# Kernel tuning notes

Hardware: AMD Instinct MI355X
Metric: run time of the kernel (lower is better)

Reference implementation:

```python
import jax, jax.numpy as jnp
import numpy as np

N_USERS = 200000
N_ITEMS = 50000
F = 64          # n_factors
B = 32768       # batch of (user, item) pairs
L = 256         # ratings per user (dense-ified ragged lists)
MIN_R = 1
MAX_R = 5


def setup_inputs() -> dict:
    key = jax.random.key(0)
    ks = jax.random.split(key, 8)
    # xavier_normal_ std = sqrt(2 / (fan_in + fan_out))
    std_u = (2.0 / (N_USERS + F)) ** 0.5
    std_i = (2.0 / (N_ITEMS + F)) ** 0.5
    user_factors = jax.random.normal(ks[0], (N_USERS, F), dtype=jnp.float32) * std_u
    item_factors = jax.random.normal(ks[1], (N_ITEMS, F), dtype=jnp.float32) * std_i
    user_biases = jax.random.normal(ks[2], (N_USERS, 1), dtype=jnp.float32)
    item_biases = jax.random.normal(ks[3], (N_ITEMS, 1), dtype=jnp.float32)
    # integer star ratings in [MIN_R, MAX_R], one dense row per user
    ratings = jax.random.randint(ks[4], (N_USERS, L), MIN_R, MAX_R + 1).astype(jnp.float32)
    users = jax.random.randint(ks[5], (B,), 0, N_USERS)
    items = jax.random.randint(ks[6], (B,), 0, N_ITEMS)
    item_pos = jax.random.randint(ks[7], (B,), 0, L)  # position of the item in the user's rating row
    return {
        "users": users, "items": items, "item_pos": item_pos,
        "ratings": ratings,
        "user_factors": user_factors, "item_factors": item_factors,
        "user_biases": user_biases, "item_biases": item_biases,
        "min_rating": MIN_R, "max_rating": MAX_R,
    }


def reference(users, items, item_pos, ratings, user_factors, item_factors,
              user_biases, item_biases, min_rating, max_rating):
    b = users.shape[0]
    # MF prediction: biases + dot(user_factor, item_factor), shape [B, 1]
    pred = (user_biases[users] + item_biases[items]
            + jnp.sum(user_factors[users] * item_factors[items], axis=1, keepdims=True))
    p = pred[:, 0]  # [B]

    # per-sample: user's rating row with this item's rating replaced by the prediction
    rows = ratings[users]                                   # [B, L]
    rows = rows.at[jnp.arange(b), item_pos].set(p)          # batched index-update

    # torch.histc(bins=max_rating, min=min_rating, max=max_rating):
    # width = (max - min) / bins; values outside [min, max] ignored; x == max -> last bin
    bins = max_rating
    width = (max_rating - min_rating) / bins
    idx = jnp.floor((rows - min_rating) / width)
    idx = jnp.where(rows == max_rating, bins - 1, idx)      # [B, L]
    in_range = (rows >= min_rating) & (rows <= max_rating)

    # end bin from rounded prediction: clip(round(p), max(min-1, 0), max-1)
    end = jnp.clip(jnp.round(p), max(min_rating - 1, 0), max_rating - 1)  # [B]

    # mass = sum(hist[0:end+1]) - 0.5 * hist[end]  == count(idx<=end) - 0.5*count(idx==end)
    le = jnp.where(in_range & (idx <= end[:, None]), 1.0, 0.0)
    eq = jnp.where(in_range & (idx == end[:, None]), 1.0, 0.0)
    mass = jnp.sum(le - 0.5 * eq, axis=1, keepdims=True)    # [B, 1]

    return jnp.stack((pred, mass), axis=1)                   # [B, 2, 1]
```

## Files before the change

### kernel.cpp

```cpp
#include <hip/hip_runtime.h>

__global__ __launch_bounds__(256) void hist_mf_kernel(
    const int*   __restrict__ users,
    const int*   __restrict__ items,
    const int*   __restrict__ item_pos,
    const float* __restrict__ ratings,
    const float* __restrict__ user_factors,
    const float* __restrict__ item_factors,
    const float* __restrict__ user_biases,
    const float* __restrict__ item_biases,
    const int*   __restrict__ minr_p,
    const int*   __restrict__ maxr_p,
    int L, int F, int B,
    float* __restrict__ out)
{
    const int wavesPerBlock = blockDim.x >> 6;
    const int wave = blockIdx.x * wavesPerBlock + (threadIdx.x >> 6);
    const int lane = threadIdx.x & 63;
    if (wave >= B) return;

    const int u   = users[wave];
    const int it  = items[wave];
    const int pos = item_pos[wave];

    const int   minr = *minr_p;
    const int   maxr = *maxr_p;
    const int   bins = maxr;
    const float fmin = (float)minr;
    const float fmax = (float)maxr;
    const float width = (float)(maxr - minr) / (float)bins;
    const float lo = (float)((minr - 1) > 0 ? (minr - 1) : 0);
    const float hi = (float)(maxr - 1);

    float d = 0.f;
    for (int f = lane; f < F; f += 64)
        d += user_factors[(size_t)u * F + f] * item_factors[(size_t)it * F + f];
    #pragma unroll
    for (int o = 32; o > 0; o >>= 1) d += __shfl_xor(d, o, 64);

    const float pred = user_biases[u] + item_biases[it] + d;
    const float end  = fminf(fmaxf(rintf(pred), lo), hi);

    const float* row = ratings + (size_t)u * L;
    float mass = 0.f;

    for (int base = 0; base < (L & ~255); base += 256) {
        float4 r4 = reinterpret_cast<const float4*>(row + base)[lane];
        float rv[4] = {r4.x, r4.y, r4.z, r4.w};
        #pragma unroll
        for (int k = 0; k < 4; ++k) {
            int j = base + lane * 4 + k;
            float r = (j == pos) ? pred : rv[k];
            bool in_range = (r >= fmin) && (r <= fmax);
            float fidx = floorf((r - fmin) / width);
            if (r == fmax) fidx = (float)(bins - 1);
            if (in_range) {
                if (fidx <= end) mass += 1.0f;
                if (fidx == end) mass -= 0.5f;
            }
        }
    }
    for (int j = (L & ~255) + lane; j < L; j += 64) {
        float r = (j == pos) ? pred : row[j];
        bool in_range = (r >= fmin) && (r <= fmax);
        float fidx = floorf((r - fmin) / width);
        if (r == fmax) fidx = (float)(bins - 1);
        if (in_range) {
            if (fidx <= end) mass += 1.0f;
            if (fidx == end) mass -= 0.5f;
        }
    }

    #pragma unroll
    for (int o = 32; o > 0; o >>= 1) mass += __shfl_xor(mass, o, 64);

    if (lane == 0) {
        out[2 * wave + 0] = pred;
        out[2 * wave + 1] = mass;
    }
}

extern "C" void kernel_launch(void* const* d_in, const int* in_sizes, int n_in,
                              void* d_out, int out_size, void* d_ws, size_t ws_size,
                              hipStream_t stream) {
    const int*   users        = (const int*)  d_in[0];
    const int*   items        = (const int*)  d_in[1];
    const int*   item_pos     = (const int*)  d_in[2];
    const float* ratings      = (const float*)d_in[3];
    const float* user_factors = (const float*)d_in[4];
    const float* item_factors = (const float*)d_in[5];
    const float* user_biases  = (const float*)d_in[6];
    const float* item_biases  = (const float*)d_in[7];
    const int*   minr_p       = (const int*)  d_in[8];
    const int*   maxr_p       = (const int*)  d_in[9];

    const int B       = in_sizes[0];
    const int N_USERS = in_sizes[6];
    const int L       = in_sizes[3] / N_USERS;
    const int F       = in_sizes[4] / N_USERS;

    float* out = (float*)d_out;

    const int block = 256;
    const int wavesPerBlock = block / 64;
    const int grid = (B + wavesPerBlock - 1) / wavesPerBlock;

    hist_mf_kernel<<<grid, block, 0, stream>>>(
        users, items, item_pos, ratings, user_factors, item_factors,
        user_biases, item_biases, minr_p, maxr_p, L, F, B, out);
}
```

Before: 18.55 us.

## Process four samples per wave with hoisted row loads and vector stores

Each 64-thread block now handles four batch elements. The first float4 chunk of all four rating rows is issued before the dot products, so several independent gathers are in flight per wave. The per-element divide becomes a multiply by the reciprocal width, and outputs are written as two float4 stores. In exchange, registers per thread grow, the grid has fewer and smaller blocks, and the tail path clamps indices.

```diff
diff --git a/kernel.cpp b/kernel.cpp
--- a/kernel.cpp
+++ b/kernel.cpp
@@ -1,6 +1,8 @@
 #include <hip/hip_runtime.h>
 
-__global__ __launch_bounds__(256) void hist_mf_kernel(
+constexpr int EPW = 4;
+
+__global__ __launch_bounds__(64) void hist_mf_kernel(
     const int*   __restrict__ users,
     const int*   __restrict__ items,
     const int*   __restrict__ item_pos,
@@ -14,69 +16,120 @@
     int L, int F, int B,
     float* __restrict__ out)
 {
-    const int wavesPerBlock = blockDim.x >> 6;
-    const int wave = blockIdx.x * wavesPerBlock + (threadIdx.x >> 6);
-    const int lane = threadIdx.x & 63;
-    if (wave >= B) return;
+    const int w    = blockIdx.x;
+    const int lane = threadIdx.x;
+    const int e0   = w * EPW;
+    if (e0 >= B) return;
 
-    const int u   = users[wave];
-    const int it  = items[wave];
-    const int pos = item_pos[wave];
+    const int minr = *minr_p, maxr = *maxr_p;
+    const int bins = maxr;
+    const float fmin  = (float)minr;
+    const float fmax  = (float)maxr;
+    const float width = (float)(maxr - minr) / (float)bins;
+    const float invw  = 1.0f / width;
+    const float lo    = (float)((minr - 1) > 0 ? minr - 1 : 0);
+    const float hi    = (float)(maxr - 1);
 
-    const int   minr = *minr_p;
-    const int   maxr = *maxr_p;
-    const int   bins = maxr;
-    const float fmin = (float)minr;
-    const float fmax = (float)maxr;
-    const float width = (float)(maxr - minr) / (float)bins;
-    const float lo = (float)((minr - 1) > 0 ? (minr - 1) : 0);
-    const float hi = (float)(maxr - 1);
+    int u[EPW], it[EPW], ps[EPW];
+    #pragma unroll
+    for (int k = 0; k < EPW; ++k) {
+        int e = min(e0 + k, B - 1);
+        u[k]  = users[e];
+        it[k] = items[e];
+        ps[k] = item_pos[e];
+    }
 
-    float d = 0.f;
-    for (int f = lane; f < F; f += 64)
-        d += user_factors[(size_t)u * F + f] * item_factors[(size_t)it * F + f];
+    const float* rowp[EPW];
     #pragma unroll
-    for (int o = 32; o > 0; o >>= 1) d += __shfl_xor(d, o, 64);
+    for (int k = 0; k < EPW; ++k) rowp[k] = ratings + (size_t)u[k] * L;
 
-    const float pred = user_biases[u] + item_biases[it] + d;
-    const float end  = fminf(fmaxf(rintf(pred), lo), hi);
+    const int nchunk = ((L & 3) == 0) ? (L >> 8) : 0;
+    float4 r4[EPW];
+    #pragma unroll
+    for (int k = 0; k < EPW; ++k)
+        r4[k] = (nchunk > 0) ? reinterpret_cast<const float4*>(rowp[k])[lane]
+                             : make_float4(0.f, 0.f, 0.f, 0.f);
 
-    const float* row = ratings + (size_t)u * L;
-    float mass = 0.f;
+    float d[EPW];
+    #pragma unroll
+    for (int k = 0; k < EPW; ++k) d[k] = 0.f;
+    for (int f = lane; f < F; f += 64) {
+        #pragma unroll
+        for (int k = 0; k < EPW; ++k)
+            d[k] += user_factors[(size_t)u[k] * F + f] *
+                    item_factors[(size_t)it[k] * F + f];
+    }
+    #pragma unroll
+    for (int o = 32; o > 0; o >>= 1) {
+        #pragma unroll
+        for (int k = 0; k < EPW; ++k) d[k] += __shfl_xor(d[k], o, 64);
+    }
 
-    for (int base = 0; base < (L & ~255); base += 256) {
-        float4 r4 = reinterpret_cast<const float4*>(row + base)[lane];
-        float rv[4] = {r4.x, r4.y, r4.z, r4.w};
+    float pred[EPW], endv[EPW], mass[EPW];
+    #pragma unroll
+    for (int k = 0; k < EPW; ++k) {
+        pred[k] = user_biases[u[k]] + item_biases[it[k]] + d[k];
+        endv[k] = fminf(fmaxf(rintf(pred[k]), lo), hi);
+        mass[k] = 0.f;
+    }
+
+    auto accum = [&](float rraw, int j, int pos, float predv, float ev, float& m) {
+        float v = (j == pos) ? predv : rraw;
+        bool in = (v >= fmin) && (v <= fmax);
+        float fidx = floorf((v - fmin) * invw);
+        if (v == fmax) fidx = (float)(bins - 1);
+        if (in) {
+            if (fidx <= ev) m += 1.0f;
+            if (fidx == ev) m -= 0.5f;
+        }
+    };
+
+    if (nchunk > 0) {
+        const int j0 = lane * 4;
         #pragma unroll
-        for (int k = 0; k < 4; ++k) {
-            int j = base + lane * 4 + k;
-            float r = (j == pos) ? pred : rv[k];
-            bool in_range = (r >= fmin) && (r <= fmax);
-            float fidx = floorf((r - fmin) / width);
-            if (r == fmax) fidx = (float)(bins - 1);
-            if (in_range) {
-                if (fidx <= end) mass += 1.0f;
-                if (fidx == end) mass -= 0.5f;
-            }
+        for (int k = 0; k < EPW; ++k) {
+            accum(r4[k].x, j0 + 0, ps[k], pred[k], endv[k], mass[k]);
+            accum(r4[k].y, j0 + 1, ps[k], pred[k], endv[k], mass[k]);
+            accum(r4[k].z, j0 + 2, ps[k], pred[k], endv[k], mass[k]);
+            accum(r4[k].w, j0 + 3, ps[k], pred[k], endv[k], mass[k]);
         }
     }
-    for (int j = (L & ~255) + lane; j < L; j += 64) {
-        float r = (j == pos) ? pred : row[j];
-        bool in_range = (r >= fmin) && (r <= fmax);
-        float fidx = floorf((r - fmin) / width);
-        if (r == fmax) fidx = (float)(bins - 1);
-        if (in_range) {
-            if (fidx <= end) mass += 1.0f;
-            if (fidx == end) mass -= 0.5f;
+    for (int c = 1; c < nchunk; ++c) {
+        const int j0 = c * 256 + lane * 4;
+        #pragma unroll
+        for (int k = 0; k < EPW; ++k) {
+            float4 q = reinterpret_cast<const float4*>(rowp[k] + c * 256)[lane];
+            accum(q.x, j0 + 0, ps[k], pred[k], endv[k], mass[k]);
+            accum(q.y, j0 + 1, ps[k], pred[k], endv[k], mass[k]);
+            accum(q.z, j0 + 2, ps[k], pred[k], endv[k], mass[k]);
+            accum(q.w, j0 + 3, ps[k], pred[k], endv[k], mass[k]);
         }
+    }
+    for (int j = (nchunk << 8) + lane; j < L; j += 64) {
+        #pragma unroll
+        for (int k = 0; k < EPW; ++k)
+            accum(rowp[k][j], j, ps[k], pred[k], endv[k], mass[k]);
     }
 
     #pragma unroll
-    for (int o = 32; o > 0; o >>= 1) mass += __shfl_xor(mass, o, 64);
+    for (int o = 32; o > 0; o >>= 1) {
+        #pragma unroll
+        for (int k = 0; k < EPW; ++k) mass[k] += __shfl_xor(mass[k], o, 64);
+    }
 
     if (lane == 0) {
-        out[2 * wave + 0] = pred;
-        out[2 * wave + 1] = mass;
+        const int nv = min(EPW, B - e0);
+        if (nv == EPW) {
+            reinterpret_cast<float4*>(out)[2 * w + 0] =
+                make_float4(pred[0], mass[0], pred[1], mass[1]);
+            reinterpret_cast<float4*>(out)[2 * w + 1] =
+                make_float4(pred[2], mass[2], pred[3], mass[3]);
+        } else {
+            for (int k = 0; k < nv; ++k) {
+                out[2 * (e0 + k) + 0] = pred[k];
+                out[2 * (e0 + k) + 1] = mass[k];
+            }
+        }
     }
 }
 
@@ -101,11 +154,8 @@
 
     float* out = (float*)d_out;
 
-    const int block = 256;
-    const int wavesPerBlock = block / 64;
-    const int grid = (B + wavesPerBlock - 1) / wavesPerBlock;
-
-    hist_mf_kernel<<<grid, block, 0, stream>>>(
+    const int grid = (B + EPW - 1) / EPW;
+    hist_mf_kernel<<<grid, 64, 0, stream>>>(
         users, items, item_pos, ratings, user_factors, item_factors,
         user_biases, item_biases, minr_p, maxr_p, L, F, B, out);
 }
```

Result: no change. 18.65 us (+0.5%).
